# Performance work log

Measured on AMD Instinct MI355X. Metric: run time of the kernel, lower is better.

Reference implementation:

```python
import jax, jax.numpy as jnp
import numpy as np

N = 16384   # total queries (= total keys here)
B = 16      # scenes
K = 1024    # keys per scene (key_batch_cnt entries)
L = 32      # local neighborhood size
D = 256     # d_model
H = 8       # nhead
DFF = 1024
LN_EPS = 1e-5


def setup_inputs() -> dict:
    key = jax.random.key(0)
    ks = jax.random.split(key, 32)
    f32 = jnp.float32

    def lin(k, o, i):
        return jax.random.normal(k, (o, i), f32) * 0.02

    idx = jax.random.randint(ks[3], (N, L), 0, K)
    invalid = jax.random.uniform(ks[4], (N, L)) < 0.1
    index_pair = jnp.where(invalid, -1, idx).astype(jnp.int32)

    inp = {
        "tgt": jax.random.normal(ks[0], (N, D), f32),
        "memory": jax.random.normal(ks[1], (N, D), f32),
        "memory_pos_emb": jax.random.normal(ks[2], (N, D), f32),
        "key_batch_cnt": jnp.full((B,), K, dtype=jnp.int32),
        "index_pair": index_pair,
        "index_pair_batch": jnp.repeat(jnp.arange(B, dtype=jnp.int32), K),
        "Wq": lin(ks[5], D, D), "bq": jnp.zeros((D,), f32),
        "Wkc": lin(ks[6], D, D), "bkc": jnp.zeros((D,), f32),
        "Wkp": lin(ks[7], D, D), "bkp": jnp.zeros((D,), f32),
        "Wv": lin(ks[8], D, D), "bv": jnp.zeros((D,), f32),
        "Wo": lin(ks[9], D, D), "bo": jnp.zeros((D,), f32),
        "W1": lin(ks[10], DFF, D), "b1": jnp.zeros((DFF,), f32),
        "W2": lin(ks[11], D, DFF), "b2": jnp.zeros((D,), f32),
        "g2": jnp.ones((D,), f32), "be2": jnp.zeros((D,), f32),
        "g3": jnp.ones((D,), f32), "be3": jnp.zeros((D,), f32),
    }
    return inp


def _ln(x, g, b):
    m = jnp.mean(x, axis=-1, keepdims=True)
    v = jnp.mean((x - m) ** 2, axis=-1, keepdims=True)
    return (x - m) * jax.lax.rsqrt(v + LN_EPS) * g + b


def reference(tgt, memory, memory_pos_emb, key_batch_cnt, index_pair,
              index_pair_batch, Wq, bq, Wkc, bkc, Wkp, bkp, Wv, bv,
              Wo, bo, W1, b1, W2, b2, g2, be2, g3, be3):
    Dh = D // H
    scale = Dh ** -0.5

    # dense projections
    q = tgt @ Wq.T + bq                              # [N, D]
    k = (memory @ Wkc.T + bkc) + (memory_pos_emb @ Wkp.T + bkp)  # content + pos
    v = memory @ Wv.T + bv

    # local-index gather: per-batch indices -> global key indices
    offsets = jnp.concatenate([jnp.zeros((1,), jnp.int32),
                               jnp.cumsum(key_batch_cnt)[:-1].astype(jnp.int32)])
    mask = index_pair < 0                            # [N, L] padded neighbors
    gidx = jnp.where(mask, 0, index_pair + offsets[index_pair_batch][:, None])

    kg = k[gidx].reshape(N, L, H, Dh)                # gathered keys  [N,L,H,Dh]
    vg = v[gidx].reshape(N, L, H, Dh)                # gathered values
    qh = q.reshape(N, H, Dh)

    attn = jnp.einsum('nhd,nlhd->nhl', qh, kg) * scale
    attn = jnp.where(mask[:, None, :], -1e9, attn)
    attn = jax.nn.softmax(attn, axis=-1)
    out = jnp.einsum('nhl,nlhd->nhd', attn, vg).reshape(N, D)
    tgt2 = out @ Wo.T + bo                           # attention out_proj

    x = _ln(tgt + tgt2, g2, be2)
    ff = jax.nn.relu(x @ W1.T + b1) @ W2.T + b2
    return _ln(x + ff, g3, be3)
```

## Files before the change

### kernel.cpp

```cpp
#include <hip/hip_runtime.h>
#include <stdint.h>

#define N_TOT 16384
#define LNEI  32
#define DM    256
#define NH    8
#define DH    32
#define DFF   1024

typedef __attribute__((ext_vector_type(8))) short  short8;
typedef __attribute__((ext_vector_type(4))) float  floatx4;
typedef __attribute__((ext_vector_type(2))) float  float2_t;
typedef __attribute__((ext_vector_type(4))) int    intx4;
typedef __attribute__((ext_vector_type(4))) unsigned short ushort4_t;
typedef __attribute__((ext_vector_type(4))) unsigned int uint4_t;

#if defined(__has_builtin)
#if __has_builtin(__builtin_amdgcn_fdot2_f32_bf16)
#define HAS_DOT2 1
#endif
#endif
#ifndef HAS_DOT2
#define HAS_DOT2 0
#endif

#if HAS_DOT2
typedef __attribute__((ext_vector_type(2))) __bf16 bf16x2_t;
#endif

static __device__ __forceinline__ float b2f(unsigned short u) {
  union { unsigned int u; float f; } x; x.u = ((unsigned int)u) << 16; return x.f;
}
static __device__ __forceinline__ unsigned short f2b(float f) {
  union { float f; unsigned int u; } x; x.f = f;
  unsigned int r = x.u + 0x7fffu + ((x.u >> 16) & 1u);
  return (unsigned short)(r >> 16);
}
static __device__ __forceinline__ float lo16(unsigned int d) {
  union { unsigned int u; float f; } x; x.u = d << 16; return x.f;
}
static __device__ __forceinline__ float hi16(unsigned int d) {
  union { unsigned int u; float f; } x; x.u = d & 0xffff0000u; return x.f;
}

#define NSEG 11
struct Seg { const float* src; unsigned short* dst; int cols; int ostride; int ooff; int begin; };
struct SegTable { Seg s[NSEG]; int total; };

__global__ __launch_bounds__(256) void cvt_all(SegTable T, float* biaskv,
                                               const float* bkc, const float* bkp,
                                               const float* bv) {
  int e = (blockIdx.x * 256 + threadIdx.x) * 4;
  if (e >= T.total) {
    int c = e - T.total;
    #pragma unroll
    for (int j = 0; j < 4; ++j, ++c)
      if (c < 512) biaskv[c] = (c < 256) ? (bkc[c] + bkp[c]) : bv[c - 256];
    return;
  }
  int si = 0;
  #pragma unroll
  for (int i = 1; i < NSEG; ++i) if (e >= T.s[i].begin) si = i;
  const Seg s = T.s[si];
  const int le = e - s.begin;
  const int row = le / s.cols;
  const int col = le - row * s.cols;
  floatx4 v = {0.f, 0.f, 0.f, 0.f};
  if (s.src) v = *(const floatx4*)(s.src + le);
  ushort4_t o;
  o.x = f2b(v[0]); o.y = f2b(v[1]); o.z = f2b(v[2]); o.w = f2b(v[3]);
  *(ushort4_t*)(s.dst + (size_t)row * s.ostride + s.ooff + col) = o;
}

static __device__ __forceinline__ void gl_lds16(const unsigned short* g, unsigned short* l) {
  __builtin_amdgcn_global_load_lds(
      (const __attribute__((address_space(1))) unsigned int*)g,
      (__attribute__((address_space(3))) unsigned int*)l, 16, 0, 0);
}

template<int BN, bool RELU>
static __device__ __forceinline__ void gemm_body(
    const unsigned short* __restrict__ A, const unsigned short* __restrict__ W,
    const float* __restrict__ bias, unsigned short* __restrict__ C,
    int Nd, int K, int lda, int m0, int n0,
    unsigned short* sA, unsigned short* sB)
{
  constexpr int BM = 128, BK = 32;
  constexpr int MI = (BN == 128) ? 4 : 2;
  constexpr int NI = 4;
  constexpr int sAh = BM * BK, sBh = BN * BK;

  const int w    = threadIdx.x >> 6;
  const int lane = threadIdx.x & 63;
  const int quad = lane >> 4;
  const int l16  = lane & 15;
  const int wrow0 = (BN == 128) ? (w >> 1) * 64 : w * 32;
  const int wcol0 = (BN == 128) ? (w & 1) * 64 : 0;

  const int aflat0 = w * 512 + lane * 8;
  const int ar0 = aflat0 >> 5, ac = aflat0 & 31;

  floatx4 acc[MI][NI] = {};

  for (int k0 = 0; k0 < K; k0 += 2 * BK) {
    __syncthreads();
    #pragma unroll
    for (int half = 0; half < 2; ++half) {
      const int kk = k0 + half * BK;
      #pragma unroll
      for (int c = 0; c < 2; ++c) {
        const int row = ar0 + c * 64;
        gl_lds16(A + (size_t)(m0 + row) * lda + kk + ac, sA + half * sAh + (c * 4 + w) * 512);
      }
      if (BN == 128) {
        #pragma unroll
        for (int c = 0; c < 2; ++c) {
          const int row = ar0 + c * 64;
          gl_lds16(W + (size_t)(n0 + row) * K + kk + ac, sB + half * sBh + (c * 4 + w) * 512);
        }
      } else {
        gl_lds16(W + (size_t)(n0 + ar0) * K + kk + ac, sB + half * sBh + w * 512);
      }
    }
    __syncthreads();

    #pragma unroll
    for (int half = 0; half < 2; ++half) {
      short8 af[MI], bf[NI];
      #pragma unroll
      for (int mi = 0; mi < MI; ++mi)
        af[mi] = *(const short8*)&sA[half * sAh + (wrow0 + mi * 16 + l16) * BK + quad * 8];
      #pragma unroll
      for (int ni = 0; ni < NI; ++ni)
        bf[ni] = *(const short8*)&sB[half * sBh + (wcol0 + ni * 16 + l16) * BK + quad * 8];
      #pragma unroll
      for (int mi = 0; mi < MI; ++mi)
        #pragma unroll
        for (int ni = 0; ni < NI; ++ni)
          acc[mi][ni] = __builtin_amdgcn_mfma_f32_16x16x32_bf16(af[mi], bf[ni], acc[mi][ni], 0, 0, 0);
    }
  }

  #pragma unroll
  for (int ni = 0; ni < NI; ++ni) {
    const int col = n0 + wcol0 + ni * 16 + l16;
    const float bvv = bias[col];
    #pragma unroll
    for (int mi = 0; mi < MI; ++mi) {
      const int row0 = m0 + wrow0 + mi * 16 + quad * 4;
      #pragma unroll
      for (int i = 0; i < 4; ++i) {
        float v = acc[mi][ni][i] + bvv;
        if (RELU) v = fmaxf(v, 0.f);
        C[(size_t)(row0 + i) * Nd + col] = f2b(v);
      }
    }
  }
}

template<int BN, bool RELU>
__global__ __launch_bounds__(256) void gemm_tile(
    const unsigned short* __restrict__ A, const unsigned short* __restrict__ W,
    const float* __restrict__ bias,
    unsigned short* __restrict__ C, int M, int Nd, int K, int lda)
{
  __shared__ unsigned short sA[2 * 128 * 32];
  __shared__ unsigned short sB[2 * BN * 32];
  gemm_body<BN, RELU>(A, W, bias, C, Nd, K, lda,
                      blockIdx.x * 128, blockIdx.y * BN, sA, sB);
}

__global__ __launch_bounds__(256) void gemm_qkv(
    const unsigned short* __restrict__ tgt_b, const unsigned short* __restrict__ Wq_b,
    const float* __restrict__ bq, unsigned short* __restrict__ q_b,
    const unsigned short* __restrict__ mp_b, const unsigned short* __restrict__ Wkv_b,
    const float* __restrict__ bias_kv, unsigned short* __restrict__ kv_b)
{
  __shared__ unsigned short sA[2 * 128 * 32];
  __shared__ unsigned short sB[2 * 64 * 32];
  const int m0 = blockIdx.x * 128;
  if (blockIdx.y < 4)
    gemm_body<64, false>(tgt_b, Wq_b, bq, q_b, 256, 256, 256,
                         m0, blockIdx.y * 64, sA, sB);
  else
    gemm_body<64, false>(mp_b, Wkv_b, bias_kv, kv_b, 512, 512, 512,
                         m0, (blockIdx.y - 4) * 64, sA, sB);
}

template<bool RES_F32, bool OUT_F32>
__global__ __launch_bounds__(256) void gemm_ln(
    const unsigned short* __restrict__ A,
    const unsigned short* __restrict__ W,
    const float* __restrict__ bias,
    const void* __restrict__ res,
    const float* __restrict__ g, const float* __restrict__ be,
    void* __restrict__ out,
    int K)
{
  constexpr int BM = 64, Nd = 256, BK = 32;
  constexpr int sAh = BM * BK, sBh = Nd * BK;
  __shared__ unsigned short sA[2 * sAh];
  __shared__ unsigned short sB[2 * sBh];

  const int t    = threadIdx.x;
  const int w    = t >> 6;
  const int lane = t & 63;
  const int quad = lane >> 4;
  const int l16  = lane & 15;
  const int m0   = blockIdx.x * BM;

  const int aflat = t * 8;
  const int ar = aflat >> 5, ac = aflat & 31;

  floatx4 acc[16] = {};

  for (int k0 = 0; k0 < K; k0 += 2 * BK) {
    __syncthreads();
    #pragma unroll
    for (int half = 0; half < 2; ++half) {
      const int kk = k0 + half * BK;
      gl_lds16(A + (size_t)(m0 + ar) * K + kk + ac, &sA[half * sAh + aflat]);
      #pragma unroll
      for (int c = 0; c < 4; ++c) {
        const int bflat = c * 2048 + t * 8;
        const int br = bflat >> 5, bc = bflat & 31;
        gl_lds16(W + (size_t)br * K + kk + bc, &sB[half * sBh + bflat]);
      }
    }
    __syncthreads();
    #pragma unroll
    for (int half = 0; half < 2; ++half) {
      const short8 af = *(const short8*)&sA[half * sAh + (w * 16 + l16) * BK + quad * 8];
      #pragma unroll
      for (int ni = 0; ni < 16; ++ni) {
        const short8 bf = *(const short8*)&sB[half * sBh + (ni * 16 + l16) * BK + quad * 8];
        acc[ni] = __builtin_amdgcn_mfma_f32_16x16x32_bf16(af, bf, acc[ni], 0, 0, 0);
      }
    }
  }

  const int row_base = m0 + w * 16 + quad * 4;
  float x[4][16];
  #pragma unroll
  for (int ni = 0; ni < 16; ++ni) {
    const int col = ni * 16 + l16;
    const float bv = bias[col];
    #pragma unroll
    for (int i = 0; i < 4; ++i) {
      float r;
      if (RES_F32) r = ((const float*)res)[(size_t)(row_base + i) * Nd + col];
      else         r = b2f(((const unsigned short*)res)[(size_t)(row_base + i) * Nd + col]);
      x[i][ni] = acc[ni][i] + bv + r;
    }
  }
  #pragma unroll
  for (int i = 0; i < 4; ++i) {
    float s = 0.f, s2 = 0.f;
    #pragma unroll
    for (int ni = 0; ni < 16; ++ni) { s += x[i][ni]; s2 += x[i][ni] * x[i][ni]; }
    #pragma unroll
    for (int msk = 8; msk >= 1; msk >>= 1) {
      s  += __shfl_xor(s, msk, 64);
      s2 += __shfl_xor(s2, msk, 64);
    }
    const float mean = s * (1.f / 256.f);
    const float var  = s2 * (1.f / 256.f) - mean * mean;
    const float rs   = rsqrtf(var + 1e-5f);
    #pragma unroll
    for (int ni = 0; ni < 16; ++ni) {
      const int col = ni * 16 + l16;
      const float y = (x[i][ni] - mean) * rs * g[col] + be[col];
      if (OUT_F32) ((float*)out)[(size_t)(row_base + i) * Nd + col] = y;
      else ((unsigned short*)out)[(size_t)(row_base + i) * Nd + col] = f2b(y);
    }
  }
}

__global__ __launch_bounds__(256) void attn_kernel(
    const unsigned short* __restrict__ q, const unsigned short* __restrict__ kv,
    const int* __restrict__ key_batch_cnt, const int* __restrict__ index_pair,
    const int* __restrict__ index_pair_batch,
    unsigned short* __restrict__ out)
{
  const int n = ((blockIdx.x & 7) << 11) | (blockIdx.x >> 3);
  const int t = threadIdx.x;
  __shared__ unsigned short s_qb[DM];
#if !HAS_DOT2
  __shared__ float s_qf[DM];
#endif
  __shared__ int   s_gidx[LNEI];
  __shared__ int   s_goff[LNEI];
  __shared__ float s_score[NH][LNEI];
  __shared__ float s_prob[NH][LNEI];
  __shared__ float s_out[2][DM];

  const unsigned short qr = q[(size_t)n * DM + t];
  s_qb[t] = qr;
#if !HAS_DOT2
  s_qf[t] = b2f(qr);
#endif
  if (t < 64) {
    const int b = index_pair_batch[n];
    int cnt = (t < 16) ? key_batch_cnt[t] : 0;
    cnt = (t < b) ? cnt : 0;
    #pragma unroll
    for (int msk = 32; msk >= 1; msk >>= 1) cnt += __shfl_xor(cnt, msk, 64);
    if (t < LNEI) {
      const int ip = index_pair[(size_t)n * LNEI + t];
      const int gi = (ip < 0) ? -1 : (ip + cnt);
      s_gidx[t] = gi;
      s_goff[t] = (gi < 0 ? 0 : gi) << 10;
    }
  }
  __syncthreads();

  {
    const int j  = t >> 3;
    const int c8 = t & 7;
    const int g  = s_gidx[j];
    const char* kbase = (const char*)kv + s_goff[j];

    float part[4];
    #pragma unroll
    for (int i = 0; i < 4; ++i) {
      const int c = c8 + i * 8;
      const uint4_t d = *(const uint4_t*)(kbase + c * 16);
#if HAS_DOT2
      union { uint4_t u; bf16x2_t p[4]; } ku, qu;
      ku.u = d;
      qu.u = *(const uint4_t*)&s_qb[c * 8];
      float acc = 0.f;
      #pragma unroll
      for (int r = 0; r < 4; ++r)
        acc = __builtin_amdgcn_fdot2_f32_bf16(ku.p[r], qu.p[r], acc, false);
      part[i] = acc;
#else
      const float* qp = &s_qf[c * 8];
      part[i] = lo16(d.x) * qp[0] + hi16(d.x) * qp[1]
              + lo16(d.y) * qp[2] + hi16(d.y) * qp[3]
              + lo16(d.z) * qp[4] + hi16(d.z) * qp[5]
              + lo16(d.w) * qp[6] + hi16(d.w) * qp[7];
#endif
    }
    #pragma unroll
    for (int i = 0; i < 4; ++i) {
      part[i] += __shfl_xor(part[i], 1, 64);
      part[i] += __shfl_xor(part[i], 2, 64);
    }
    if ((c8 & 3) == 0) {
      const int hodd = c8 >> 2;
      #pragma unroll
      for (int i = 0; i < 4; ++i)
        s_score[2 * i + hodd][j] =
            (g < 0) ? -1e9f : part[i] * 0.17677669529663687f;
    }
  }
  __syncthreads();

  {
    const int h = t >> 5;
    const int l = t & 31;
    const float sc = s_score[h][l];
    float mx = sc;
    #pragma unroll
    for (int msk = 16; msk >= 1; msk >>= 1) mx = fmaxf(mx, __shfl_xor(mx, msk, 64));
    const float e = __expf(sc - mx);
    float sm = e;
    #pragma unroll
    for (int msk = 16; msk >= 1; msk >>= 1) sm += __shfl_xor(sm, msk, 64);
    s_prob[h][l] = e / sm;
  }
  __syncthreads();

  {
    const int jh  = t >> 7;
    const int h   = (t >> 4) & 7;
    const int dh2 = t & 15;
    floatx4 p4[4];
    intx4   o4[4];
    #pragma unroll
    for (int r = 0; r < 4; ++r) {
      p4[r] = *(const floatx4*)&s_prob[h][jh * 16 + r * 4];
      o4[r] = *(const intx4*)&s_goff[jh * 16 + r * 4];
    }
    float2_t acc = {0.f, 0.f};
    const char* vbase = (const char*)kv + 512 + h * 64 + dh2 * 4;
    #pragma unroll
    for (int j2 = 0; j2 < 16; ++j2) {
      const int off = o4[j2 >> 2][j2 & 3];
      const float p = p4[j2 >> 2][j2 & 3];
      const unsigned int d = *(const unsigned int*)(vbase + off);
      acc = __builtin_elementwise_fma((float2_t){p, p},
                                      (float2_t){lo16(d), hi16(d)}, acc);
    }
    s_out[jh][h * DH + dh2 * 2]     = acc[0];
    s_out[jh][h * DH + dh2 * 2 + 1] = acc[1];
  }
  __syncthreads();

  out[(size_t)n * DM + t] = f2b(s_out[0][t] + s_out[1][t]);
}

extern "C" void kernel_launch(void* const* d_in, const int* in_sizes, int n_in,
                              void* d_out, int out_size, void* d_ws, size_t ws_size,
                              hipStream_t stream) {
  const float* tgt  = (const float*)d_in[0];
  const float* mem  = (const float*)d_in[1];
  const float* pos  = (const float*)d_in[2];
  const int* kbc    = (const int*)d_in[3];
  const int* ipair  = (const int*)d_in[4];
  const int* ipb    = (const int*)d_in[5];
  const float* Wq   = (const float*)d_in[6];
  const float* bq   = (const float*)d_in[7];
  const float* Wkc  = (const float*)d_in[8];
  const float* bkc  = (const float*)d_in[9];
  const float* Wkp  = (const float*)d_in[10];
  const float* bkp  = (const float*)d_in[11];
  const float* Wv   = (const float*)d_in[12];
  const float* bvp  = (const float*)d_in[13];
  const float* Wo   = (const float*)d_in[14];
  const float* bo   = (const float*)d_in[15];
  const float* W1   = (const float*)d_in[16];
  const float* b1   = (const float*)d_in[17];
  const float* W2   = (const float*)d_in[18];
  const float* b2   = (const float*)d_in[19];
  const float* g2   = (const float*)d_in[20];
  const float* be2  = (const float*)d_in[21];
  const float* g3   = (const float*)d_in[22];
  const float* be3  = (const float*)d_in[23];

  const size_t NB = (size_t)N_TOT * DM;
  unsigned short* ws = (unsigned short*)d_ws;
  unsigned short* tgt_b = ws;
  unsigned short* ao_b  = ws;
  unsigned short* mp_b  = ws + 2 * NB;
  unsigned short* x_b   = ws + 2 * NB;
  unsigned short* q_b   = ws + 4 * NB;
  unsigned short* h1_b  = ws + 4 * NB;
  unsigned short* kv_b  = ws + 5 * NB;
  unsigned short* wgt   = ws + 8 * NB;
  unsigned short* Wq_b  = wgt;
  unsigned short* Wkv_b = wgt + 65536;
  unsigned short* Wo_b  = wgt + 65536 + 262144;
  unsigned short* W1_b  = wgt + 2 * 65536 + 262144;
  unsigned short* W2_b  = wgt + 2 * 65536 + 2 * 262144;
  float* bias_kv = (float*)(wgt + 2 * 65536 + 3 * 262144);

  SegTable T;
  int beg = 0, i = 0;
  auto seg = [&](const float* s, unsigned short* d, int cols, int ostride, int ooff, int nelem) {
    T.s[i].src = s; T.s[i].dst = d; T.s[i].cols = cols;
    T.s[i].ostride = ostride; T.s[i].ooff = ooff; T.s[i].begin = beg;
    beg += nelem; ++i;
  };
  seg(tgt, tgt_b, DM, DM, 0,   (int)NB);
  seg(mem, mp_b,  DM, 512, 0,  (int)NB);
  seg(pos, mp_b,  DM, 512, DM, (int)NB);
  seg(Wq,  Wq_b,  DM, DM, 0,   65536);
  seg(Wkc, Wkv_b, DM, 512, 0,  65536);
  seg(Wkp, Wkv_b, DM, 512, DM, 65536);
  seg(Wv,  Wkv_b + (size_t)256 * 512, DM, 512, 0, 65536);
  seg(nullptr, Wkv_b + (size_t)256 * 512, DM, 512, DM, 65536);
  seg(Wo,  Wo_b,  DM, DM, 0,   65536);
  seg(W1,  W1_b,  DM, DM, 0,   262144);
  seg(W2,  W2_b,  DFF, DFF, 0, 262144);
  T.total = beg;

  dim3 blk(256);
  cvt_all<<<dim3(T.total / 1024 + 1), blk, 0, stream>>>(T, bias_kv, bkc, bkp, bvp);

  dim3 gQKV(N_TOT / 128, 12);
  dim3 gF(N_TOT / 128, DFF / 128);
  dim3 gLN(N_TOT / 64);

  gemm_qkv<<<gQKV, blk, 0, stream>>>(tgt_b, Wq_b, bq, q_b, mp_b, Wkv_b, bias_kv, kv_b);
  attn_kernel<<<dim3(N_TOT), blk, 0, stream>>>(q_b, kv_b, kbc, ipair, ipb, ao_b);
  gemm_ln<true, false><<<gLN, blk, 0, stream>>>(ao_b, Wo_b, bo, tgt, g2, be2, x_b, DM);
  gemm_tile<128, true><<<gF, blk, 0, stream>>>(x_b, W1_b, b1, h1_b, N_TOT, DFF, DM, DM);
  gemm_ln<false, true><<<gLN, blk, 0, stream>>>(h1_b, W2_b, b2, x_b, g3, be3, d_out, DFF);
}
```

Measured before the change: 260.0 us.

## Split gemm_ln across 8 waves with cross-wave LayerNorm reduction; widen KV tiles

The fused GEMM+LayerNorm kernel now runs 512 threads (8 waves), each wave owning a 16x128 half-row tile instead of a full 16x256 row. Row statistics are combined across the two column halves through a small shared-memory reduction and an extra barrier. This halves per-wave accumulator registers and spreads the B-tile loads over more threads, aiming for better occupancy and latency hiding. Separately, the KV projection part of gemm_qkv uses 128-wide N tiles, so the grid shrinks from 12 to 8 column blocks at the cost of doubling that kernel's sB shared-memory buffer.

```diff
diff --git a/kernel.cpp b/kernel.cpp
--- a/kernel.cpp
+++ b/kernel.cpp
@@ -177,18 +177,18 @@
     const float* __restrict__ bias_kv, unsigned short* __restrict__ kv_b)
 {
   __shared__ unsigned short sA[2 * 128 * 32];
-  __shared__ unsigned short sB[2 * 64 * 32];
+  __shared__ unsigned short sB[2 * 128 * 32];
   const int m0 = blockIdx.x * 128;
   if (blockIdx.y < 4)
     gemm_body<64, false>(tgt_b, Wq_b, bq, q_b, 256, 256, 256,
                          m0, blockIdx.y * 64, sA, sB);
   else
-    gemm_body<64, false>(mp_b, Wkv_b, bias_kv, kv_b, 512, 512, 512,
-                         m0, (blockIdx.y - 4) * 64, sA, sB);
+    gemm_body<128, false>(mp_b, Wkv_b, bias_kv, kv_b, 512, 512, 512,
+                         m0, (blockIdx.y - 4) * 128, sA, sB);
 }
 
 template<bool RES_F32, bool OUT_F32>
-__global__ __launch_bounds__(256) void gemm_ln(
+__global__ __launch_bounds__(512) void gemm_ln(
     const unsigned short* __restrict__ A,
     const unsigned short* __restrict__ W,
     const float* __restrict__ bias,
@@ -201,6 +201,7 @@
   constexpr int sAh = BM * BK, sBh = Nd * BK;
   __shared__ unsigned short sA[2 * sAh];
   __shared__ unsigned short sB[2 * sBh];
+  __shared__ float s_red[2][BM][2];
 
   const int t    = threadIdx.x;
   const int w    = t >> 6;
@@ -208,70 +209,90 @@
   const int quad = lane >> 4;
   const int l16  = lane & 15;
   const int m0   = blockIdx.x * BM;
-
-  const int aflat = t * 8;
-  const int ar = aflat >> 5, ac = aflat & 31;
-
-  floatx4 acc[16] = {};
+  const int wr   = (w >> 1) * 16;
+  const int wc   = (w & 1) * 128;
+
+  floatx4 acc[8] = {};
 
   for (int k0 = 0; k0 < K; k0 += 2 * BK) {
     __syncthreads();
     #pragma unroll
     for (int half = 0; half < 2; ++half) {
       const int kk = k0 + half * BK;
-      gl_lds16(A + (size_t)(m0 + ar) * K + kk + ac, &sA[half * sAh + aflat]);
-      #pragma unroll
-      for (int c = 0; c < 4; ++c) {
-        const int bflat = c * 2048 + t * 8;
-        const int br = bflat >> 5, bc = bflat & 31;
-        gl_lds16(W + (size_t)br * K + kk + bc, &sB[half * sBh + bflat]);
+      if (t < 256) {
+        const int aflat = t * 8;
+        gl_lds16(A + (size_t)(m0 + (aflat >> 5)) * K + kk + (aflat & 31),
+                 &sA[half * sAh + aflat]);
       }
+      #pragma unroll
+      for (int c = 0; c < 2; ++c) {
+        const int bflat = c * 4096 + t * 8;
+        gl_lds16(W + (size_t)(bflat >> 5) * K + kk + (bflat & 31),
+                 &sB[half * sBh + bflat]);
+      }
     }
     __syncthreads();
     #pragma unroll
     for (int half = 0; half < 2; ++half) {
-      const short8 af = *(const short8*)&sA[half * sAh + (w * 16 + l16) * BK + quad * 8];
-      #pragma unroll
-      for (int ni = 0; ni < 16; ++ni) {
-        const short8 bf = *(const short8*)&sB[half * sBh + (ni * 16 + l16) * BK + quad * 8];
+      const short8 af = *(const short8*)&sA[half * sAh + (wr + l16) * BK + quad * 8];
+      #pragma unroll
+      for (int ni = 0; ni < 8; ++ni) {
+        const short8 bf = *(const short8*)&sB[half * sBh + (wc + ni * 16 + l16) * BK + quad * 8];
         acc[ni] = __builtin_amdgcn_mfma_f32_16x16x32_bf16(af, bf, acc[ni], 0, 0, 0);
       }
     }
   }
 
-  const int row_base = m0 + w * 16 + quad * 4;
-  float x[4][16];
+  const int rl0 = wr + quad * 4;
+  float x[4][8];
   #pragma unroll
-  for (int ni = 0; ni < 16; ++ni) {
-    const int col = ni * 16 + l16;
+  for (int ni = 0; ni < 8; ++ni) {
+    const int col = wc + ni * 16 + l16;
     const float bv = bias[col];
     #pragma unroll
     for (int i = 0; i < 4; ++i) {
+      const size_t idx = (size_t)(m0 + rl0 + i) * Nd + col;
       float r;
-      if (RES_F32) r = ((const float*)res)[(size_t)(row_base + i) * Nd + col];
-      else         r = b2f(((const unsigned short*)res)[(size_t)(row_base + i) * Nd + col]);
+      if (RES_F32) r = ((const float*)res)[idx];
+      else         r = b2f(((const unsigned short*)res)[idx]);
       x[i][ni] = acc[ni][i] + bv + r;
     }
   }
+  float ps[4], ps2[4];
   #pragma unroll
   for (int i = 0; i < 4; ++i) {
     float s = 0.f, s2 = 0.f;
     #pragma unroll
-    for (int ni = 0; ni < 16; ++ni) { s += x[i][ni]; s2 += x[i][ni] * x[i][ni]; }
+    for (int ni = 0; ni < 8; ++ni) { s += x[i][ni]; s2 += x[i][ni] * x[i][ni]; }
     #pragma unroll
     for (int msk = 8; msk >= 1; msk >>= 1) {
       s  += __shfl_xor(s, msk, 64);
       s2 += __shfl_xor(s2, msk, 64);
     }
+    ps[i] = s; ps2[i] = s2;
+  }
+  if (l16 == 0) {
+    #pragma unroll
+    for (int i = 0; i < 4; ++i) {
+      s_red[w & 1][rl0 + i][0] = ps[i];
+      s_red[w & 1][rl0 + i][1] = ps2[i];
+    }
+  }
+  __syncthreads();
+  #pragma unroll
+  for (int i = 0; i < 4; ++i) {
+    const float s    = s_red[0][rl0 + i][0] + s_red[1][rl0 + i][0];
+    const float s2   = s_red[0][rl0 + i][1] + s_red[1][rl0 + i][1];
     const float mean = s * (1.f / 256.f);
     const float var  = s2 * (1.f / 256.f) - mean * mean;
     const float rs   = rsqrtf(var + 1e-5f);
     #pragma unroll
-    for (int ni = 0; ni < 16; ++ni) {
-      const int col = ni * 16 + l16;
+    for (int ni = 0; ni < 8; ++ni) {
+      const int col = wc + ni * 16 + l16;
       const float y = (x[i][ni] - mean) * rs * g[col] + be[col];
-      if (OUT_F32) ((float*)out)[(size_t)(row_base + i) * Nd + col] = y;
-      else ((unsigned short*)out)[(size_t)(row_base + i) * Nd + col] = f2b(y);
+      const size_t idx = (size_t)(m0 + rl0 + i) * Nd + col;
+      if (OUT_F32) ((float*)out)[idx] = y;
+      else ((unsigned short*)out)[idx] = f2b(y);
     }
   }
 }
@@ -469,13 +490,13 @@
   dim3 blk(256);
   cvt_all<<<dim3(T.total / 1024 + 1), blk, 0, stream>>>(T, bias_kv, bkc, bkp, bvp);
 
-  dim3 gQKV(N_TOT / 128, 12);
+  dim3 gQKV(N_TOT / 128, 8);
   dim3 gF(N_TOT / 128, DFF / 128);
   dim3 gLN(N_TOT / 64);
 
   gemm_qkv<<<gQKV, blk, 0, stream>>>(tgt_b, Wq_b, bq, q_b, mp_b, Wkv_b, bias_kv, kv_b);
   attn_kernel<<<dim3(N_TOT), blk, 0, stream>>>(q_b, kv_b, kbc, ipair, ipb, ao_b);
-  gemm_ln<true, false><<<gLN, blk, 0, stream>>>(ao_b, Wo_b, bo, tgt, g2, be2, x_b, DM);
+  gemm_ln<true, false><<<gLN, dim3(512), 0, stream>>>(ao_b, Wo_b, bo, tgt, g2, be2, x_b, DM);
   gemm_tile<128, true><<<gF, blk, 0, stream>>>(x_b, W1_b, b1, h1_b, N_TOT, DFF, DM, DM);
-  gemm_ln<false, true><<<gLN, blk, 0, stream>>>(h1_b, W2_b, b2, x_b, g3, be3, d_out, DFF);
-}
+  gemm_ln<false, true><<<gLN, dim3(512), 0, stream>>>(h1_b, W2_b, b2, x_b, g3, be3, d_out, DFF);
+}
```

Measured after the change: 258.5 us. Within noise of the previous version (-0.6%).
